# Optimization experiments

Hardware: AMD Instinct MI355X
Metric: run time of the kernel (lower is better)

The kernel has to match this reference:

```python
import jax, jax.numpy as jnp
import numpy as np

N = 50000      # nodes
F = 128        # in_features
OUT = 128      # out_features
E = 600000     # edges per adjacency (avg degree 12)
J = 2
BN_EPS = 1e-5


def setup_inputs() -> dict:
    key = jax.random.key(0)
    ks = jax.random.split(key, 10)
    x = jax.random.normal(ks[0], (N, F), dtype=jnp.float32)
    rows0 = jax.random.randint(ks[1], (E,), 0, N, dtype=jnp.int32)
    cols0 = jax.random.randint(ks[2], (E,), 0, N, dtype=jnp.int32)
    vals0 = jax.random.uniform(ks[3], (E,), dtype=jnp.float32)
    rows1 = jax.random.randint(ks[4], (E,), 0, N, dtype=jnp.int32)
    cols1 = jax.random.randint(ks[5], (E,), 0, N, dtype=jnp.int32)
    vals1 = jax.random.uniform(ks[6], (E,), dtype=jnp.float32)
    # Linear(J*F, OUT) params, torch default init U(-1/sqrt(fan_in), 1/sqrt(fan_in))
    lim = 1.0 / np.sqrt(J * F)
    W_fc = jax.random.uniform(ks[7], (OUT, J * F), dtype=jnp.float32, minval=-lim, maxval=lim)
    b_fc = jax.random.uniform(ks[8], (OUT,), dtype=jnp.float32, minval=-lim, maxval=lim)
    gamma = jnp.ones((OUT,), dtype=jnp.float32)
    beta = jnp.zeros((OUT,), dtype=jnp.float32)
    return {"x": x, "rows0": rows0, "cols0": cols0, "vals0": vals0,
            "rows1": rows1, "cols1": cols1, "vals1": vals1,
            "W_fc": W_fc, "b_fc": b_fc, "gamma": gamma, "beta": beta}


def _spmm(rows, cols, vals, x):
    # sparse [N,N] @ dense [N,F]: gather source features, weight, scatter-add to rows
    msgs = vals[:, None] * x[cols]                      # [E, F]
    return jax.ops.segment_sum(msgs, rows, num_segments=x.shape[0])  # [N, F]


def reference(x, rows0, cols0, vals0, rows1, cols1, vals1, W_fc, b_fc, gamma, beta):
    h = jnp.concatenate([_spmm(rows0, cols0, vals0, x),
                         _spmm(rows1, cols1, vals1, x)], axis=1)  # [N, J*F]
    y = h @ W_fc.T + b_fc                                         # [N, OUT]
    # BatchNorm1d (training mode: batch stats, biased variance)
    mean = jnp.mean(y, axis=0)
    var = jnp.mean((y - mean) ** 2, axis=0)
    return (y - mean) * jax.lax.rsqrt(var + BN_EPS) * gamma + beta
```

## Files before the change

### kernel.cpp

```cpp
#include <hip/hip_runtime.h>

#define N_NODES 50000
#define F_IN 128
#define OUT_F 128
#define JF 256
#define EDGES 600000
#define BN_EPS 1e-5f
#define MAXDEG 48

#define SCAT_B 4688
#define CONVX_B 6250
#define CONVW_B 32
#define BUILD_B (SCAT_B + CONVX_B + CONVW_B)
#define FUSE_B 3125
#define NCOPY 16

typedef __attribute__((ext_vector_type(8))) short short8;
typedef __attribute__((ext_vector_type(4))) float floatx4;
typedef __attribute__((ext_vector_type(4))) unsigned short ushortx4;

static __device__ __forceinline__ unsigned short f2bf(float f) {
    unsigned int x = __float_as_uint(f);
    unsigned int r = (x + 0x7fffu + ((x >> 16) & 1u)) >> 16;
    return (unsigned short)r;
}
static __device__ __forceinline__ float bflo(unsigned int p) { return __uint_as_float(p << 16); }
static __device__ __forceinline__ float bfhi(unsigned int p) { return __uint_as_float(p & 0xffff0000u); }

__global__ __launch_bounds__(256) void build_kernel(
    const int* __restrict__ rows0, const int* __restrict__ cols0, const float* __restrict__ vals0,
    const int* __restrict__ rows1, const int* __restrict__ cols1, const float* __restrict__ vals1,
    int* __restrict__ cnt0, int* __restrict__ cnt1,
    unsigned int* __restrict__ pe0, unsigned int* __restrict__ pe1,
    const floatx4* __restrict__ x4, ushortx4* __restrict__ xb4,
    const floatx4* __restrict__ W4, ushortx4* __restrict__ Wb4)
{
    int bid = blockIdx.x;
    int tid = threadIdx.x;
    if (bid < SCAT_B) {
        int t = bid * 256 + tid;
        if (t < EDGES) {
            int r = __builtin_nontemporal_load(rows0 + t);
            int c = __builtin_nontemporal_load(cols0 + t);
            float v = __builtin_nontemporal_load(vals0 + t);
            int p = atomicAdd(&cnt0[r], 1);
            if (p < MAXDEG)
                pe0[p * N_NODES + r] = ((unsigned int)c << 16) | f2bf(v);
        } else if (t < 2 * EDGES) {
            int e = t - EDGES;
            int r = __builtin_nontemporal_load(rows1 + e);
            int c = __builtin_nontemporal_load(cols1 + e);
            float v = __builtin_nontemporal_load(vals1 + e);
            int p = atomicAdd(&cnt1[r], 1);
            if (p < MAXDEG)
                pe1[p * N_NODES + r] = ((unsigned int)c << 16) | f2bf(v);
        }
    } else if (bid < SCAT_B + CONVX_B) {
        int i = (bid - SCAT_B) * 256 + tid;
        floatx4 v = __builtin_nontemporal_load(&x4[i]);
        ushortx4 o;
        o.x = f2bf(v.x); o.y = f2bf(v.y); o.z = f2bf(v.z); o.w = f2bf(v.w);
        __builtin_nontemporal_store(o, &xb4[i]);
    } else {
        int i = (bid - SCAT_B - CONVX_B) * 256 + tid;
        floatx4 v = W4[i];
        ushortx4 o;
        o.x = f2bf(v.x); o.y = f2bf(v.y); o.z = f2bf(v.z); o.w = f2bf(v.w);
        Wb4[i] = o;
    }
}

__global__ __launch_bounds__(256) void gather_gemm(
    const unsigned int* __restrict__ xb32,
    const int* __restrict__ cnt0, const unsigned int* __restrict__ pe0,
    const int* __restrict__ cnt1, const unsigned int* __restrict__ pe1,
    const ushort* __restrict__ Wb, const float* __restrict__ bias,
    float* __restrict__ y, float* __restrict__ stats)
{
    __shared__ unsigned int hsu[16 * 128];
    __shared__ float lstat[256];

    int tid = threadIdx.x;
    int lane = tid & 63;
    int w = tid >> 6;
    int wu = __builtin_amdgcn_readfirstlane(w);
    int row0 = blockIdx.x * 16;

    lstat[tid] = 0.f;

    for (int rr = 0; rr < 4; ++rr) {
        int lr = wu * 4 + rr;
        int r = row0 + lr;
        float aL0 = 0.f, aL1 = 0.f, aR0 = 0.f, aR1 = 0.f;

        {
            int deg = cnt0[r]; if (deg > MAXDEG) deg = MAXDEG;
            const unsigned int* qp = pe0 + r;
            int p = 0;
            for (; p + 4 <= deg; p += 4) {
                unsigned int qa = qp[(p + 0) * N_NODES];
                unsigned int qb = qp[(p + 1) * N_NODES];
                unsigned int qc = qp[(p + 2) * N_NODES];
                unsigned int qd = qp[(p + 3) * N_NODES];
                unsigned int x0 = xb32[(qa >> 16) * 64 + lane];
                unsigned int x1 = xb32[(qb >> 16) * 64 + lane];
                unsigned int x2 = xb32[(qc >> 16) * 64 + lane];
                unsigned int x3 = xb32[(qd >> 16) * 64 + lane];
                float v0 = __uint_as_float(qa << 16), v1 = __uint_as_float(qb << 16);
                float v2 = __uint_as_float(qc << 16), v3 = __uint_as_float(qd << 16);
                aL0 += v0 * bflo(x0) + v1 * bflo(x1) + v2 * bflo(x2) + v3 * bflo(x3);
                aL1 += v0 * bfhi(x0) + v1 * bfhi(x1) + v2 * bfhi(x2) + v3 * bfhi(x3);
            }
            for (; p < deg; ++p) {
                unsigned int q = qp[p * N_NODES];
                unsigned int xv = xb32[(q >> 16) * 64 + lane];
                float v = __uint_as_float(q << 16);
                aL0 += v * bflo(xv); aL1 += v * bfhi(xv);
            }
        }
        {
            int deg = cnt1[r]; if (deg > MAXDEG) deg = MAXDEG;
            const unsigned int* qp = pe1 + r;
            int p = 0;
            for (; p + 4 <= deg; p += 4) {
                unsigned int qa = qp[(p + 0) * N_NODES];
                unsigned int qb = qp[(p + 1) * N_NODES];
                unsigned int qc = qp[(p + 2) * N_NODES];
                unsigned int qd = qp[(p + 3) * N_NODES];
                unsigned int x0 = xb32[(qa >> 16) * 64 + lane];
                unsigned int x1 = xb32[(qb >> 16) * 64 + lane];
                unsigned int x2 = xb32[(qc >> 16) * 64 + lane];
                unsigned int x3 = xb32[(qd >> 16) * 64 + lane];
                float v0 = __uint_as_float(qa << 16), v1 = __uint_as_float(qb << 16);
                float v2 = __uint_as_float(qc << 16), v3 = __uint_as_float(qd << 16);
                aR0 += v0 * bflo(x0) + v1 * bflo(x1) + v2 * bflo(x2) + v3 * bflo(x3);
                aR1 += v0 * bfhi(x0) + v1 * bfhi(x1) + v2 * bfhi(x2) + v3 * bfhi(x3);
            }
            for (; p < deg; ++p) {
                unsigned int q = qp[p * N_NODES];
                unsigned int xv = xb32[(q >> 16) * 64 + lane];
                float v = __uint_as_float(q << 16);
                aR0 += v * bflo(xv); aR1 += v * bfhi(xv);
            }
        }

        unsigned int sw = (unsigned int)((lr & 7) << 4);
        unsigned int offL = ((unsigned int)(lr * 512 + lane * 4)) ^ sw;
        unsigned int offR = ((unsigned int)(lr * 512 + 256 + lane * 4)) ^ sw;
        *(unsigned int*)((char*)hsu + offL) =
            (unsigned int)f2bf(aL0) | ((unsigned int)f2bf(aL1) << 16);
        *(unsigned int*)((char*)hsu + offR) =
            (unsigned int)f2bf(aR0) | ((unsigned int)f2bf(aR1) << 16);
    }
    __syncthreads();

    floatx4 acc[2];
    acc[0] = (floatx4){0.f, 0.f, 0.f, 0.f};
    acc[1] = (floatx4){0.f, 0.f, 0.f, 0.f};

    int colb = lane & 15;
    int kg = lane >> 4;
    unsigned int asw = (unsigned int)((colb & 7) << 4);
    const char* hbase = (const char*)hsu;
    const ushort* wp = Wb + (size_t)(w * 32 + colb) * JF + kg * 8;

    #pragma unroll
    for (int k0 = 0; k0 < 8; ++k0) {
        unsigned int aoff = ((unsigned int)(colb * 512 + k0 * 64 + kg * 16)) ^ asw;
        short8 a = *(const short8*)(hbase + aoff);
        #pragma unroll
        for (int c = 0; c < 2; ++c) {
            short8 b = *(const short8*)(wp + c * 16 * JF + k0 * 32);
            acc[c] = __builtin_amdgcn_mfma_f32_16x16x32_bf16(a, b, acc[c], 0, 0, 0);
        }
    }

    int rq = kg * 4;
    #pragma unroll
    for (int c = 0; c < 2; ++c) {
        int col = w * 32 + c * 16 + colb;
        float bv = bias[col];
        float s = 0.f, s2 = 0.f;
        #pragma unroll
        for (int q = 0; q < 4; ++q) {
            float val = acc[c][q] + bv;
            y[(size_t)(row0 + rq + q) * OUT_F + col] = val;
            s += val; s2 += val * val;
        }
        atomicAdd(&lstat[col], s);
        atomicAdd(&lstat[128 + col], s2);
    }
    __syncthreads();
    float* sdst = stats + (size_t)(blockIdx.x & (NCOPY - 1)) * 256;
    atomicAdd(&sdst[tid], lstat[tid]);
}

__global__ void bn_prep(const float* __restrict__ stats,
                        const float* __restrict__ gamma,
                        const float* __restrict__ beta,
                        float* __restrict__ ss)
{
    int o = threadIdx.x;
    if (o >= OUT_F) return;
    float s = 0.f, s2 = 0.f;
    #pragma unroll
    for (int c = 0; c < NCOPY; ++c) {
        s  += stats[c * 256 + o];
        s2 += stats[c * 256 + 128 + o];
    }
    float inv_n = 1.0f / (float)N_NODES;
    float mean = s * inv_n;
    float var  = s2 * inv_n - mean * mean;
    float sc = rsqrtf(var + BN_EPS) * gamma[o];
    ss[o] = sc;
    ss[OUT_F + o] = beta[o] - mean * sc;
}

__global__ __launch_bounds__(256) void bn_apply(
    float* __restrict__ y, const float* __restrict__ ss)
{
    size_t i = (size_t)blockIdx.x * blockDim.x + threadIdx.x;
    size_t total = (size_t)N_NODES * OUT_F / 4;
    if (i >= total) return;

    int c4 = (int)(i & (OUT_F / 4 - 1));
    float4 v  = ((const float4*)y)[i];
    float4 sc = ((const float4*)ss)[c4];
    float4 sh = ((const float4*)(ss + OUT_F))[c4];
    v.x = v.x * sc.x + sh.x;
    v.y = v.y * sc.y + sh.y;
    v.z = v.z * sc.z + sh.z;
    v.w = v.w * sc.w + sh.w;
    ((float4*)y)[i] = v;
}

extern "C" void kernel_launch(void* const* d_in, const int* in_sizes, int n_in,
                              void* d_out, int out_size, void* d_ws, size_t ws_size,
                              hipStream_t stream)
{
    const float* x     = (const float*)d_in[0];
    const int*   rows0 = (const int*)  d_in[1];
    const int*   cols0 = (const int*)  d_in[2];
    const float* vals0 = (const float*)d_in[3];
    const int*   rows1 = (const int*)  d_in[4];
    const int*   cols1 = (const int*)  d_in[5];
    const float* vals1 = (const float*)d_in[6];
    const float* W     = (const float*)d_in[7];
    const float* b     = (const float*)d_in[8];
    const float* gamma = (const float*)d_in[9];
    const float* beta  = (const float*)d_in[10];

    float* y = (float*)d_out;

    ushort* xb = (ushort*)d_ws;
    ushort* Wb = xb + (size_t)N_NODES * F_IN;
    unsigned int* pe0 = (unsigned int*)(Wb + OUT_F * JF);
    unsigned int* pe1 = pe0 + (size_t)MAXDEG * N_NODES;
    int* cnt0 = (int*)(pe1 + (size_t)MAXDEG * N_NODES);
    int* cnt1 = cnt0 + N_NODES;
    float* stats = (float*)(cnt1 + N_NODES);
    float* ss    = stats + NCOPY * 256;

    hipMemsetAsync(cnt0, 0, (2 * (size_t)N_NODES + NCOPY * 256) * sizeof(int), stream);

    build_kernel<<<BUILD_B, 256, 0, stream>>>(
        rows0, cols0, vals0, rows1, cols1, vals1,
        cnt0, cnt1, pe0, pe1,
        (const floatx4*)x, (ushortx4*)xb, (const floatx4*)W, (ushortx4*)Wb);

    gather_gemm<<<FUSE_B, 256, 0, stream>>>(
        (const unsigned int*)xb, cnt0, pe0, cnt1, pe1, Wb, b, y, stats);

    bn_prep<<<1, 128, 0, stream>>>(stats, gamma, beta, ss);
    bn_apply<<<CONVX_B, 256, 0, stream>>>(y, ss);
}
```

Measured before the change: 165.6 us.

## Use row-major padded edge lists with row-partitioned scatter and vectorized record loads

The per-row edge slot array moves from slot-major (p*N + r) to row-major (r*MAXDEG + p), so gather_gemm can fetch the first 24 records of a row as six uint4 loads and finish any remainder in a scalar loop. The scatter phase becomes 8 row partitions times 2048-edge chunks. Each block reads a chunk with int4 loads and keeps only the edges whose row falls in its partition, which localizes the atomics and writes into a smaller address window. The cost is that every row index is read 8 times, and the scatter grid and instruction count grow. The gather always loads 24 records per row even when the degree is about 12, adding wasted load bandwidth.

```diff
diff --git a/kernel.cpp b/kernel.cpp
--- a/kernel.cpp
+++ b/kernel.cpp
@@ -7,8 +7,12 @@
 #define EDGES 600000
 #define BN_EPS 1e-5f
 #define MAXDEG 48
-
-#define SCAT_B 4688
+#define NPART 8
+#define PART_ROWS 6250
+#define CHUNK_E 2048
+#define NCHUNK 586
+
+#define SCAT_B (NPART * NCHUNK)
 #define CONVX_B 6250
 #define CONVW_B 32
 #define BUILD_B (SCAT_B + CONVX_B + CONVW_B)
@@ -38,22 +42,54 @@
     int bid = blockIdx.x;
     int tid = threadIdx.x;
     if (bid < SCAT_B) {
-        int t = bid * 256 + tid;
-        if (t < EDGES) {
-            int r = __builtin_nontemporal_load(rows0 + t);
-            int c = __builtin_nontemporal_load(cols0 + t);
-            float v = __builtin_nontemporal_load(vals0 + t);
-            int p = atomicAdd(&cnt0[r], 1);
-            if (p < MAXDEG)
-                pe0[p * N_NODES + r] = ((unsigned int)c << 16) | f2bf(v);
-        } else if (t < 2 * EDGES) {
-            int e = t - EDGES;
-            int r = __builtin_nontemporal_load(rows1 + e);
-            int c = __builtin_nontemporal_load(cols1 + e);
-            float v = __builtin_nontemporal_load(vals1 + e);
-            int p = atomicAdd(&cnt1[r], 1);
-            if (p < MAXDEG)
-                pe1[p * N_NODES + r] = ((unsigned int)c << 16) | f2bf(v);
+        unsigned part = (unsigned)(bid & (NPART - 1));
+        int c0 = (bid >> 3) * CHUNK_E;
+
+        bool pure0 = (c0 + CHUNK_E <= EDGES);
+        bool pure1 = (c0 >= EDGES) && (c0 + CHUNK_E <= 2 * EDGES);
+        if (pure0 || pure1) {
+            const int*   rows = pure1 ? rows1 : rows0;
+            const int*   cols = pure1 ? cols1 : cols0;
+            const float* vals = pure1 ? vals1 : vals0;
+            int*          cnt = pure1 ? cnt1 : cnt0;
+            unsigned int*  pe = pure1 ? pe1 : pe0;
+            int eb = pure1 ? c0 - EDGES : c0;
+            #pragma unroll
+            for (int g = 0; g < 2; ++g) {
+                int e = eb + g * 1024 + tid * 4;
+                int4 rv = *(const int4*)(rows + e);
+                int rr[4] = {rv.x, rv.y, rv.z, rv.w};
+                #pragma unroll
+                for (int j = 0; j < 4; ++j) {
+                    int r = rr[j];
+                    if ((unsigned)r / (unsigned)PART_ROWS == part) {
+                        int ee = e + j;
+                        int c = cols[ee];
+                        float v = vals[ee];
+                        int p = atomicAdd(&cnt[r], 1);
+                        if (p < MAXDEG)
+                            pe[(size_t)r * MAXDEG + p] = ((unsigned int)c << 16) | f2bf(v);
+                    }
+                }
+            }
+        } else {
+            for (int i = 0; i < CHUNK_E / 256; ++i) {
+                int e = c0 + i * 256 + tid;
+                if (e < 2 * EDGES) {
+                    bool s1 = e >= EDGES;
+                    int ee = s1 ? e - EDGES : e;
+                    int r = s1 ? rows1[ee] : rows0[ee];
+                    if ((unsigned)r / (unsigned)PART_ROWS == part) {
+                        int c = s1 ? cols1[ee] : cols0[ee];
+                        float v = s1 ? vals1[ee] : vals0[ee];
+                        int* cnt = s1 ? cnt1 : cnt0;
+                        unsigned int* pe = s1 ? pe1 : pe0;
+                        int p = atomicAdd(&cnt[r], 1);
+                        if (p < MAXDEG)
+                            pe[(size_t)r * MAXDEG + p] = ((unsigned int)c << 16) | f2bf(v);
+                    }
+                }
+            }
         }
     } else if (bid < SCAT_B + CONVX_B) {
         int i = (bid - SCAT_B) * 256 + tid;
@@ -70,6 +106,18 @@
     }
 }
 
+static __device__ __forceinline__ void rec_acc(
+    unsigned int q, bool on, int lane,
+    const unsigned int* __restrict__ xb32, float& A0, float& A1)
+{
+    unsigned int idx = q >> 16;
+    if (idx > (unsigned)(N_NODES - 1)) idx = N_NODES - 1;
+    float vv = on ? __uint_as_float(q << 16) : 0.0f;
+    unsigned int xv = xb32[idx * 64 + lane];
+    A0 += vv * bflo(xv);
+    A1 += vv * bfhi(xv);
+}
+
 __global__ __launch_bounds__(256) void gather_gemm(
     const unsigned int* __restrict__ xb32,
     const int* __restrict__ cnt0, const unsigned int* __restrict__ pe0,
@@ -91,58 +139,40 @@
     for (int rr = 0; rr < 4; ++rr) {
         int lr = wu * 4 + rr;
         int r = row0 + lr;
+
+        int d0 = cnt0[r]; if (d0 > MAXDEG) d0 = MAXDEG;
+        int d1 = cnt1[r]; if (d1 > MAXDEG) d1 = MAXDEG;
+        const uint4* q0 = (const uint4*)(pe0 + (size_t)r * MAXDEG);
+        const uint4* q1 = (const uint4*)(pe1 + (size_t)r * MAXDEG);
+
+        uint4 ra[6], rb[6];
+        #pragma unroll
+        for (int i = 0; i < 6; ++i) { ra[i] = q0[i]; rb[i] = q1[i]; }
+
         float aL0 = 0.f, aL1 = 0.f, aR0 = 0.f, aR1 = 0.f;
 
-        {
-            int deg = cnt0[r]; if (deg > MAXDEG) deg = MAXDEG;
-            const unsigned int* qp = pe0 + r;
-            int p = 0;
-            for (; p + 4 <= deg; p += 4) {
-                unsigned int qa = qp[(p + 0) * N_NODES];
-                unsigned int qb = qp[(p + 1) * N_NODES];
-                unsigned int qc = qp[(p + 2) * N_NODES];
-                unsigned int qd = qp[(p + 3) * N_NODES];
-                unsigned int x0 = xb32[(qa >> 16) * 64 + lane];
-                unsigned int x1 = xb32[(qb >> 16) * 64 + lane];
-                unsigned int x2 = xb32[(qc >> 16) * 64 + lane];
-                unsigned int x3 = xb32[(qd >> 16) * 64 + lane];
-                float v0 = __uint_as_float(qa << 16), v1 = __uint_as_float(qb << 16);
-                float v2 = __uint_as_float(qc << 16), v3 = __uint_as_float(qd << 16);
-                aL0 += v0 * bflo(x0) + v1 * bflo(x1) + v2 * bflo(x2) + v3 * bflo(x3);
-                aL1 += v0 * bfhi(x0) + v1 * bfhi(x1) + v2 * bfhi(x2) + v3 * bfhi(x3);
+        #pragma unroll
+        for (int g = 0; g < 6; ++g) {
+            if (g * 4 < d0) {
+                rec_acc(ra[g].x, g * 4 + 0 < d0, lane, xb32, aL0, aL1);
+                rec_acc(ra[g].y, g * 4 + 1 < d0, lane, xb32, aL0, aL1);
+                rec_acc(ra[g].z, g * 4 + 2 < d0, lane, xb32, aL0, aL1);
+                rec_acc(ra[g].w, g * 4 + 3 < d0, lane, xb32, aL0, aL1);
             }
-            for (; p < deg; ++p) {
-                unsigned int q = qp[p * N_NODES];
-                unsigned int xv = xb32[(q >> 16) * 64 + lane];
-                float v = __uint_as_float(q << 16);
-                aL0 += v * bflo(xv); aL1 += v * bfhi(xv);
+        }
+        #pragma unroll
+        for (int g = 0; g < 6; ++g) {
+            if (g * 4 < d1) {
+                rec_acc(rb[g].x, g * 4 + 0 < d1, lane, xb32, aR0, aR1);
+                rec_acc(rb[g].y, g * 4 + 1 < d1, lane, xb32, aR0, aR1);
+                rec_acc(rb[g].z, g * 4 + 2 < d1, lane, xb32, aR0, aR1);
+                rec_acc(rb[g].w, g * 4 + 3 < d1, lane, xb32, aR0, aR1);
             }
         }
-        {
-            int deg = cnt1[r]; if (deg > MAXDEG) deg = MAXDEG;
-            const unsigned int* qp = pe1 + r;
-            int p = 0;
-            for (; p + 4 <= deg; p += 4) {
-                unsigned int qa = qp[(p + 0) * N_NODES];
-                unsigned int qb = qp[(p + 1) * N_NODES];
-                unsigned int qc = qp[(p + 2) * N_NODES];
-                unsigned int qd = qp[(p + 3) * N_NODES];
-                unsigned int x0 = xb32[(qa >> 16) * 64 + lane];
-                unsigned int x1 = xb32[(qb >> 16) * 64 + lane];
-                unsigned int x2 = xb32[(qc >> 16) * 64 + lane];
-                unsigned int x3 = xb32[(qd >> 16) * 64 + lane];
-                float v0 = __uint_as_float(qa << 16), v1 = __uint_as_float(qb << 16);
-                float v2 = __uint_as_float(qc << 16), v3 = __uint_as_float(qd << 16);
-                aR0 += v0 * bflo(x0) + v1 * bflo(x1) + v2 * bflo(x2) + v3 * bflo(x3);
-                aR1 += v0 * bfhi(x0) + v1 * bfhi(x1) + v2 * bfhi(x2) + v3 * bfhi(x3);
-            }
-            for (; p < deg; ++p) {
-                unsigned int q = qp[p * N_NODES];
-                unsigned int xv = xb32[(q >> 16) * 64 + lane];
-                float v = __uint_as_float(q << 16);
-                aR0 += v * bflo(xv); aR1 += v * bfhi(xv);
-            }
-        }
+        for (int p = 24; p < d0; ++p)
+            rec_acc(pe0[(size_t)r * MAXDEG + p], true, lane, xb32, aL0, aL1);
+        for (int p = 24; p < d1; ++p)
+            rec_acc(pe1[(size_t)r * MAXDEG + p], true, lane, xb32, aR0, aR1);
 
         unsigned int sw = (unsigned int)((lr & 7) << 4);
         unsigned int offL = ((unsigned int)(lr * 512 + lane * 4)) ^ sw;
@@ -255,8 +285,8 @@
     ushort* xb = (ushort*)d_ws;
     ushort* Wb = xb + (size_t)N_NODES * F_IN;
     unsigned int* pe0 = (unsigned int*)(Wb + OUT_F * JF);
-    unsigned int* pe1 = pe0 + (size_t)MAXDEG * N_NODES;
-    int* cnt0 = (int*)(pe1 + (size_t)MAXDEG * N_NODES);
+    unsigned int* pe1 = pe0 + (size_t)N_NODES * MAXDEG;
+    int* cnt0 = (int*)(pe1 + (size_t)N_NODES * MAXDEG);
     int* cnt1 = cnt0 + N_NODES;
     float* stats = (float*)(cnt1 + N_NODES);
     float* ss    = stats + NCOPY * 256;
```

Measured after the change: 162.0 us. 1.02x faster.
